# Optimization experiments

Measured on AMD Instinct MI355X. Metric: run time of the kernel, lower is better.

## Reference

```python
import jax, jax.numpy as jnp
import numpy as np
from functools import partial

IMAGE_SIZE = 256
ORIG_SIZE = 1024
NEAR, FAR = 0.1, 100.0
CHUNK = 100  # faces processed per scan step to bound memory


def setup_inputs():
    key = jax.random.key(0)
    kv, kf = jax.random.split(key)
    B, V, F = 4, 5000, 10000
    verts = jax.random.normal(kv, (B, V, 3), jnp.float32) * 0.4
    verts = verts.at[..., 2].add(2.5)  # object in front of camera (+z)
    faces = jax.random.randint(kf, (B, F, 3), 0, V)
    fx = fy = float(ORIG_SIZE)
    cx = cy = ORIG_SIZE / 2.0
    K = jnp.broadcast_to(jnp.array([[fx, 0., cx], [0., fy, cy], [0., 0., 1.]], jnp.float32), (B, 3, 3))
    R = jnp.broadcast_to(jnp.eye(3, dtype=jnp.float32), (B, 3, 3))
    t = jnp.zeros((B, 1, 3), jnp.float32)
    dist_coeffs = jnp.zeros((B, 5), jnp.float32)
    return {"vertices": verts, "faces": faces, "K": K, "R": R, "t": t, "dist_coeffs": dist_coeffs}


def projection(vertices, K, R, t, dist_coeffs, orig_size, eps=1e-9):
    # vertices: [B,V,3]; matmul(vertices, R^T) + t, OpenCV distortion, intrinsics, NDC
    v = jnp.einsum('bvj,bij->bvi', vertices, R) + t
    x, y, z = v[..., 0], v[..., 1], v[..., 2]
    x_ = x / (z + eps)
    y_ = y / (z + eps)
    k1, k2, p1, p2, k3 = [dist_coeffs[:, i:i + 1] for i in range(5)]
    r2 = x_ * x_ + y_ * y_
    rad = 1. + k1 * r2 + k2 * r2 * r2 + k3 * r2 * r2 * r2
    x__ = x_ * rad + 2. * p1 * x_ * y_ + p2 * (r2 + 2. * x_ * x_)
    y__ = y_ * rad + p1 * (r2 + 2. * y_ * y_) + 2. * p2 * x_ * y_
    vv = jnp.stack([x__, y__, jnp.ones_like(z)], axis=-1)
    vv = jnp.einsum('bvj,bij->bvi', vv, K)
    u, vc = vv[..., 0], vv[..., 1]
    vc = orig_size - vc  # image y points down
    u = 2. * (u - orig_size / 2.) / orig_size
    vc = 2. * (vc - orig_size / 2.) / orig_size
    return jnp.stack([u, vc, z], axis=-1)  # [B,V,3] in NDC xy, camera z


def vertices_to_faces(vertices, faces):
    # vertices [B,V,3], faces [B,F,3] -> [B,F,3,3]
    return jnp.take_along_axis(vertices[:, :, None, :], faces[:, :, :, None], axis=1)


def rasterize_depth(face_verts, image_size, near, far):
    # face_verts: [B,F,3,3]; z-buffer min of barycentric-interpolated 1/z depth
    B, F = face_verts.shape[:2]
    pad = (-F) % CHUNK
    fv = jnp.pad(face_verts, ((0, 0), (0, pad), (0, 0), (0, 0)))  # padded faces are degenerate
    n_chunks = (F + pad) // CHUNK
    fv = fv.reshape(B, n_chunks, CHUNK, 3, 3).transpose(1, 0, 2, 3, 4)  # [n,B,C,3,3]
    ps = (2. * jnp.arange(image_size, dtype=jnp.float32) + 1. - image_size) / image_size
    xp = ps[None, None, None, :]  # [1,1,1,W]
    yp = ps[None, None, :, None]  # [1,1,H,1]
    eps = 1e-8

    def step(zbuf, chunk):  # chunk [B,C,3,3]
        x = chunk[..., 0]
        y = chunk[..., 1]
        z = chunk[..., 2]
        x0, x1, x2 = (x[..., i, None, None] for i in range(3))
        y0, y1, y2 = (y[..., i, None, None] for i in range(3))
        z0, z1, z2 = (z[..., i, None, None] for i in range(3))
        denom = (y1 - y2) * (x0 - x2) + (x2 - x1) * (y0 - y2)
        ok = jnp.abs(denom) > eps
        safe_d = jnp.where(ok, denom, 1.)
        w0 = ((y1 - y2) * (xp - x2) + (x2 - x1) * (yp - y2)) / safe_d  # [B,C,H,W]
        w1 = ((y2 - y0) * (xp - x2) + (x0 - x2) * (yp - y2)) / safe_d
        w2 = 1. - w0 - w1
        inside = (w0 >= 0.) & (w1 >= 0.) & (w2 >= 0.) & ok
        zs0 = jnp.where(z0 > eps, z0, 1.)
        zs1 = jnp.where(z1 > eps, z1, 1.)
        zs2 = jnp.where(z2 > eps, z2, 1.)
        zinv = w0 / zs0 + w1 / zs1 + w2 / zs2
        zp = 1. / jnp.where(zinv > eps, zinv, 1.)
        valid = inside & (zp > near) & (zp < far) & (z0 > eps) & (z1 > eps) & (z2 > eps)
        zp = jnp.where(valid, zp, far)
        zbuf = jnp.minimum(zbuf, jnp.min(zp, axis=1))  # min over faces in chunk
        return zbuf, None

    zbuf0 = jnp.full((B, image_size, image_size), far, dtype=face_verts.dtype)
    zbuf, _ = jax.lax.scan(step, zbuf0, fv)
    return zbuf[:, ::-1, :]  # flip vertically to image convention


def reference(vertices, faces, K, R, t, dist_coeffs):
    # fill_back: append faces with reversed winding
    faces_fb = jnp.concatenate([faces, faces[:, :, ::-1]], axis=1)
    v_ndc = projection(vertices, K, R, t, dist_coeffs, float(ORIG_SIZE))
    fverts = vertices_to_faces(v_ndc, faces_fb)  # [B,2F,3,3]
    return rasterize_depth(fverts, IMAGE_SIZE, NEAR, FAR)  # [B,H,W] depth map
```

## Files before the change

### kernel.cpp

```cpp
#include <hip/hip_runtime.h>

#define IMG 256
#define TW 32
#define TH 32
#define TILES 64
#define SUBSPLIT 16
#define RSUB 8
#define BIGF 1e30f

typedef float v4f __attribute__((ext_vector_type(4)));

__device__ __forceinline__ float ndc(int i) { return (2.0f*i + 1.0f - IMG) * (1.0f/IMG); }

__device__ __forceinline__ void rank_to_tile(int rank, int& tx, int& ty) {
    int k, base;
    if (rank < 4)       { k = 0; base = 0;  }
    else if (rank < 16) { k = 1; base = 4;  }
    else if (rank < 36) { k = 2; base = 16; }
    else                { k = 3; base = 36; }
    int j = rank - base;
    int s = 2*k + 2;
    int seg = j / (s - 1);
    int off = j - seg * (s - 1);
    int lo = 3 - k, hi = 4 + k;
    if      (seg == 0) { tx = lo + off; ty = lo; }
    else if (seg == 1) { tx = hi;       ty = lo + off; }
    else if (seg == 2) { tx = hi - off; ty = hi; }
    else               { tx = lo;       ty = hi - off; }
}

__device__ __forceinline__ bool tile_test(v4f gx, v4f gy, v4f a,
                                          float txlo, float txhi, float tylo, float tyhi) {
    float m0 = fmaxf(gx.x*txlo, gx.x*txhi) + fmaxf(gy.x*tylo, gy.x*tyhi) + a.x;
    float m1 = fmaxf(gx.y*txlo, gx.y*txhi) + fmaxf(gy.y*tylo, gy.y*tyhi) + a.y;
    float m2 = fmaxf(gx.z*txlo, gx.z*txhi) + fmaxf(gy.z*tylo, gy.z*tyhi) + a.z;
    return fminf(fminf(m0, m1), m2) >= -1e-5f;
}

__device__ __forceinline__ float plane_min(float gw, float hw, float aw,
                                           float xlo, float xhi, float ylo, float yhi) {
    return fminf(gw*xlo, gw*xhi) + fminf(hw*ylo, hw*yhi) + aw;
}

__device__ __forceinline__ float wave_max_dpp(float v) {
    int x;
    x = __builtin_amdgcn_update_dpp(0, __float_as_int(v), 0x111, 0xF, 0xF, true);
    v = fmaxf(v, __int_as_float(x));
    x = __builtin_amdgcn_update_dpp(0, __float_as_int(v), 0x112, 0xF, 0xF, true);
    v = fmaxf(v, __int_as_float(x));
    x = __builtin_amdgcn_update_dpp(0, __float_as_int(v), 0x114, 0xF, 0xF, true);
    v = fmaxf(v, __int_as_float(x));
    x = __builtin_amdgcn_update_dpp(0, __float_as_int(v), 0x118, 0xF, 0xF, true);
    v = fmaxf(v, __int_as_float(x));
    x = __builtin_amdgcn_update_dpp(0, __float_as_int(v), 0x142, 0xF, 0xF, true);
    v = fmaxf(v, __int_as_float(x));
    x = __builtin_amdgcn_update_dpp(0, __float_as_int(v), 0x143, 0xF, 0xF, true);
    v = fmaxf(v, __int_as_float(x));
    return __int_as_float(__builtin_amdgcn_readlane(__float_as_int(v), 63));
}

__device__ __forceinline__ unsigned long long cover_mask_px(int i0, int i1, int j0, int j1,
                                                            v4f gx, v4f gy, v4f aa) {
    if (i0 > 255 || i1 < 0 || j0 > 255 || j1 < 0) return 0ull;
    int tx0 = max(i0, 0) >> 5, tx1 = min(i1, 255) >> 5;
    int ty0 = max(j0, 0) >> 5, ty1 = min(j1, 255) >> 5;
    unsigned long long m = 0ull;
    for (int ty = ty0; ty <= ty1; ++ty) {
        float tylo = ndc(ty*TH), tyhi = ndc(ty*TH + TH - 1);
        for (int tx = tx0; tx <= tx1; ++tx) {
            if (tile_test(gx, gy, aa, ndc(tx*TW), ndc(tx*TW + TW - 1), tylo, tyhi))
                m |= 1ull << (ty*8 + tx);
        }
    }
    return m;
}

__global__ void k_prep(const float* __restrict__ verts, const int* __restrict__ faces,
                       const float* __restrict__ Km, const float* __restrict__ Rm,
                       const float* __restrict__ tm, const float* __restrict__ dm,
                       v4f* __restrict__ fd, v4f* __restrict__ bb,
                       unsigned int* __restrict__ ids,
                       unsigned int* __restrict__ outz, unsigned int* __restrict__ gcnt,
                       int B, int V, int F, int nz, int faceBlocks, int doBins) {
    if ((int)blockIdx.x >= faceBlocks) {
        int idx = (blockIdx.x - faceBlocks) * 256 + threadIdx.x;
        int stride = (gridDim.x - faceBlocks) * 256;
        for (int j = idx; j < nz; j += stride) outz[j] = 0x42C80000u;
        return;
    }
    __shared__ int lcnt[1024];
    __shared__ unsigned int lbase[1024];
    __shared__ int lofs[1024];
    int nbins = TILES * B;
    int tid = threadIdx.x;
    if (doBins) {
        for (int k = tid; k < nbins; k += 256) { lcnt[k] = 0; lofs[k] = 0; }
        __syncthreads();
    }
    int i = blockIdx.x * 256 + tid;
    bool alive = i < B * F;
    unsigned long long tmask = 0ull;
    int b = 0, j0c = 0, j1c = 0;
    if (alive) {
        b = i / F;
        const float* vb = verts + (size_t)b * V * 3;
        const float* R = Rm + b * 9;
        const float* K = Km + b * 9;
        const float* t = tm + b * 3;
        const float* d = dm + b * 5;
        float X[3], Y[3], Z[3];
        #pragma unroll
        for (int c = 0; c < 3; ++c) {
            int vi = faces[3*i + c];
            float px = vb[3*vi], py = vb[3*vi+1], pz = vb[3*vi+2];
            float x = R[0]*px + R[1]*py + R[2]*pz + t[0];
            float y = R[3]*px + R[4]*py + R[5]*pz + t[1];
            float z = R[6]*px + R[7]*py + R[8]*pz + t[2];
            float iz = 1.0f / (z + 1e-9f);
            float x_ = x * iz, y_ = y * iz;
            float k1 = d[0], k2 = d[1], p1 = d[2], p2 = d[3], k3 = d[4];
            float r2 = x_*x_ + y_*y_;
            float rad = 1.0f + k1*r2 + k2*r2*r2 + k3*r2*r2*r2;
            float xd = x_*rad + 2.0f*p1*x_*y_ + p2*(r2 + 2.0f*x_*x_);
            float yd = y_*rad + p1*(r2 + 2.0f*y_*y_) + 2.0f*p2*x_*y_;
            float u  = K[0]*xd + K[1]*yd + K[2];
            float vc = K[3]*xd + K[4]*yd + K[5];
            vc = 1024.0f - vc;
            X[c] = (u  - 512.0f) * (1.0f/512.0f);
            Y[c] = (vc - 512.0f) * (1.0f/512.0f);
            Z[c] = z;
        }
        float x0=X[0], y0=Y[0], z0=Z[0], x1=X[1], y1=Y[1], z1=Z[1], x2=X[2], y2=Y[2], z2=Z[2];
        float denom = (y1-y2)*(x0-x2) + (x2-x1)*(y0-y2);
        bool ok = (fabsf(denom) > 1e-8f) && (z0 > 1e-8f) && (z1 > 1e-8f) && (z2 > 1e-8f);
        if (!ok) {
            bb[i] = (v4f){3e38f, -3e38f, 3e38f, -3e38f};
        } else {
            float s = (denom > 0.0f) ? 1.0f : -1.0f;
            float absd = fabsf(denom);
            float P0x = s*(y1-y2), P0y = s*(x2-x1);
            float P1x = s*(y2-y0), P1y = s*(x0-x2);
            float P2x = -(P0x + P1x), P2y = -(P0y + P1y);
            float A0 = -(P0x*x2 + P0y*y2);
            float A1 = -(P1x*x2 + P1y*y2);
            float A2 = absd - A0 - A1;
            float ia  = 1.0f / absd;
            float rz0 = ia / z0, rz1 = ia / z1, rz2 = ia / z2;
            float zix = P0x*rz0 + P1x*rz1 + P2x*rz2;
            float ziy = P0y*rz0 + P1y*rz1 + P2y*rz2;
            float zic = A0*rz0 + A1*rz1 + A2*rz2;
            v4f ga = (v4f){P0x, P1x, P2x, -zix};
            v4f gb = (v4f){P0y, P1y, P2y, -ziy};
            v4f gc = (v4f){A0,  A1,  A2,  10.0f - zic};
            fd[(size_t)i*3 + 0] = ga;
            fd[(size_t)i*3 + 1] = gb;
            fd[(size_t)i*3 + 2] = gc;
            float xmn = fminf(x0, fminf(x1, x2)) - 1e-4f;
            float xmx = fmaxf(x0, fmaxf(x1, x2)) + 1e-4f;
            float ymn = fminf(y0, fminf(y1, y2)) - 1e-4f;
            float ymx = fmaxf(y0, fmaxf(y1, y2)) + 1e-4f;
            bb[i] = (v4f){xmn, xmx, ymn, ymx};
            if (doBins) {
                int i0 = (int)floorf(xmn*128.0f + 127.5f);
                int i1 = (int)ceilf (xmx*128.0f + 127.5f);
                int j0 = (int)floorf(ymn*128.0f + 127.5f);
                int j1 = (int)ceilf (ymx*128.0f + 127.5f);
                tmask = cover_mask_px(i0, i1, j0, j1, ga, gb, gc);
                j0c = max(j0, 0); j1c = min(j1, 255);
            }
        }
    }
    if (doBins) {
        unsigned long long mk = tmask;
        while (mk) {
            int t = __builtin_ctzll(mk); mk &= mk - 1ull;
            atomicAdd(&lcnt[t*B + b], 1);
        }
        __syncthreads();
        for (int k = tid; k < nbins; k += 256)
            if (lcnt[k]) lbase[k] = atomicAdd(&gcnt[k], (unsigned int)lcnt[k]);
        __syncthreads();
        mk = tmask;
        while (mk) {
            int t = __builtin_ctzll(mk); mk &= mk - 1ull;
            int ty = t >> 3;
            int bin = t*B + b;
            unsigned int blo = (unsigned int)max((j0c >> 3) - ty*4, 0);
            unsigned int bhi = (unsigned int)min((j1c >> 3) - ty*4, 3);
            unsigned int pack = (unsigned int)i | (blo << 28) | (bhi << 30);
            int sl = atomicAdd(&lofs[bin], 1);
            ids[(size_t)bin*F + lbase[bin] + sl] = pack;
        }
    }
}

__global__ __launch_bounds__(256) void k_raster(const v4f* __restrict__ fd,
                                                const unsigned int* __restrict__ ids,
                                                const unsigned int* __restrict__ gcnt,
                                                unsigned int* __restrict__ outz,
                                                int B, int F) {
    __shared__ v4f sA[257], sB[257], sC[257];
    int tid = threadIdx.x, lane = tid & 63, wave = tid >> 6;
    int wbase = wave << 6;
    int tbIdx = blockIdx.x >> 3;
    int sub = blockIdx.x & (RSUB-1);
    int rank = tbIdx / B;
    int b = tbIdx - rank * B;
    int tx, ty;
    rank_to_tile(rank, tx, ty);
    int bin = (ty*8 + tx)*B + b;
    unsigned int len = gcnt[bin];
    size_t base = (size_t)bin * F;
    unsigned int p0 = (unsigned int)(((unsigned long long)sub     * len) / RSUB);
    unsigned int p1 = (unsigned int)(((unsigned long long)(sub+1) * len) / RSUB);

    int rowbase = ty*TH + wave*8;
    int row = rowbase + (lane >> 3);
    int col = tx*TW + (lane & 7) * 4;
    float yp = ndc(row);
    float xp[4];
    #pragma unroll
    for (int jj = 0; jj < 4; ++jj) xp[jj] = ndc(col + jj);
    float txlo = ndc(tx*TW), txhi = ndc(tx*TW + TW - 1);
    float bylo = ndc(rowbase), byhi = ndc(rowbase + 7);
    float m[4] = {BIGF, BIGF, BIGF, BIGF};

    int orow = IMG - 1 - row;
    size_t zo = (size_t)b * (IMG*IMG) + (size_t)orow * IMG + col;

    float hs = 0.0f;
    #pragma unroll
    for (int jj = 0; jj < 4; ++jj) {
        float d = __uint_as_float(outz[zo + jj]);
        hs = fmaxf(hs, 10.0f - 1.0f/d);
    }
    float h = fminf(9.99f, wave_max_dpp(hs) + 1e-4f);

    if (p1 > p0) {
        unsigned int pc = ids[base + min(p0 + lane, p1 - 1)];
        bool vc = (p0 + lane) < p1;
        unsigned int pn = ids[base + min(p0 + 64 + lane, p1 - 1)];
        bool vn = (p0 + 64 + lane) < p1;

        for (unsigned int p = p0; p < p1; p += 64) {
            unsigned int p2w = ids[base + min(p + 128 + lane, p1 - 1)];
            bool v2 = (p + 128 + lane) < p1;

            unsigned int blo = (pc >> 28) & 3u, bhi = pc >> 30;
            unsigned int idc = pc & 0x0FFFFFFFu;
            bool pass = vc & ((int)blo <= wave) & ((int)bhi >= wave);
            bool full = false;
            v4f ra = (v4f){0,0,0,0}, rb = (v4f){0,0,0,0}, rc = (v4f){0,0,0,0};
            if (pass) {
                ra = fd[(size_t)idc*3]; rb = fd[(size_t)idc*3+1]; rc = fd[(size_t)idc*3+2];
                float p0l=ra.x*txlo, p0h=ra.x*txhi, q0l=rb.x*bylo, q0h=rb.x*byhi;
                float p1l=ra.y*txlo, p1h=ra.y*txhi, q1l=rb.y*bylo, q1h=rb.y*byhi;
                float p2l=ra.z*txlo, p2h=ra.z*txhi, q2l=rb.z*bylo, q2h=rb.z*byhi;
                float c0x = fmaxf(p0l,p0h) + fmaxf(q0l,q0h) + rc.x;
                float c1x = fmaxf(p1l,p1h) + fmaxf(q1l,q1h) + rc.y;
                float c2x = fmaxf(p2l,p2h) + fmaxf(q2l,q2h) + rc.z;
                float c0n = fminf(p0l,p0h) + fminf(q0l,q0h) + rc.x;
                float c1n = fminf(p1l,p1h) + fminf(q1l,q1h) + rc.y;
                float c2n = fminf(p2l,p2h) + fminf(q2l,q2h) + rc.z;
                float zmn = fminf(ra.w*txlo, ra.w*txhi) + fminf(rb.w*bylo, rb.w*byhi) + rc.w;
                pass = (fminf(fminf(c0x, c1x), c2x) >= -1e-5f) & (zmn < h);
                full = (fminf(fminf(c0n, c1n), c2n) >= 1e-5f);
            }
            unsigned long long mp = __ballot(pass && !full);
            unsigned long long mf = __ballot(pass && full);
            int cp = __popcll(mp);
            int cf = __popcll(mf);
            if (pass && !full) {
                int sl = wbase + __popcll(mp & ((1ull << lane) - 1ull));
                sA[sl] = ra; sB[sl] = rb; sC[sl] = rc;
            }
            unsigned long long w = mf;
            while (w) {
                int l = __builtin_amdgcn_readfirstlane(__ffsll((unsigned long long)w) - 1);
                w &= w - 1ull;
                float gxw = __int_as_float(__builtin_amdgcn_readlane(__float_as_int(ra.w), l));
                float gyw = __int_as_float(__builtin_amdgcn_readlane(__float_as_int(rb.w), l));
                float aaw = __int_as_float(__builtin_amdgcn_readlane(__float_as_int(rc.w), l));
                float e3 = fmaf(gyw, yp, aaw);
                #pragma unroll
                for (int jj = 0; jj < 4; ++jj)
                    m[jj] = fminf(m[jj], fmaf(gxw, xp[jj], e3));
            }
            if (cp > 0) {
                v4f gx = sA[wbase], gy = sB[wbase], aa = sC[wbase];
                for (int i = 0; i < cp; ++i) {
                    v4f nx = sA[wbase+i+1], ny = sB[wbase+i+1], nzv = sC[wbase+i+1];
                    float e0 = fmaf(gy.x, yp, aa.x);
                    float e1 = fmaf(gy.y, yp, aa.y);
                    float e2 = fmaf(gy.z, yp, aa.z);
                    float e3 = fmaf(gy.w, yp, aa.w);
                    #pragma unroll
                    for (int jj = 0; jj < 4; ++jj) {
                        float n0 = fmaf(gx.x, xp[jj], e0);
                        float n1 = fmaf(gx.y, xp[jj], e1);
                        float n2 = fmaf(gx.z, xp[jj], e2);
                        float n3 = fmaf(gx.w, xp[jj], e3);
                        float q = fminf(fminf(n0, n1), n2);
                        m[jj] = fminf(m[jj], (q >= 0.0f) ? n3 : BIGF);
                    }
                    gx = nx; gy = ny; aa = nzv;
                }
            }
            if (cp + cf > 0)
                h = fminf(9.99f, wave_max_dpp(fmaxf(fmaxf(m[0], m[1]), fmaxf(m[2], m[3]))));
            pc = pn; vc = vn;
            pn = p2w; vn = v2;
        }
    }
    #pragma unroll
    for (int jj = 0; jj < 4; ++jj) {
        if (m[jj] < 9.99f) {
            float depth = 1.0f / (10.0f - m[jj]);
            unsigned int mv = __float_as_uint(depth);
            unsigned int cv = outz[zo + jj];
            if (mv < cv) atomicMin(&outz[zo + jj], mv);
        }
    }
}

__global__ __launch_bounds__(256) void k_raster_scan(const v4f* __restrict__ fd,
                                                     const v4f* __restrict__ bb,
                                                     unsigned int* __restrict__ outz,
                                                     int B, int F) {
    __shared__ v4f sA[257], sB[257], sC[257];
    int tid = threadIdx.x, lane = tid & 63, wave = tid >> 6;
    int wbase = wave << 6;
    int j = blockIdx.x >> 4;
    int s = blockIdx.x & (SUBSPLIT-1);
    int nTB = TILES * B;
    int f_begin = (s * F) / SUBSPLIT, f_end = ((s + 1) * F) / SUBSPLIT;

    #pragma unroll 1
    for (int phase = 0; phase < 2; ++phase) {
        int tb = (phase == 0) ? j : (nTB - 1 - j);
        int rank = tb / B;
        int b = tb - rank * B;
        int tx, ty;
        rank_to_tile(rank, tx, ty);
        int rowbase = ty*TH + wave*8;
        int row = rowbase + (lane >> 3);
        int col = tx*TW + (lane & 7) * 4;
        float yp = ndc(row);
        float xp[4];
        #pragma unroll
        for (int jj = 0; jj < 4; ++jj) xp[jj] = ndc(col + jj);
        float txlo = ndc(tx*TW), txhi = ndc(tx*TW + TW - 1);
        float bylo = ndc(rowbase), byhi = ndc(rowbase + 7);
        float m[4] = {BIGF, BIGF, BIGF, BIGF};
        float h = 9.99f;

        const v4f* bbp = bb + (size_t)b * F;
        const v4f* fdp = fd + (size_t)b * F * 3;

        v4f box = bbp[min(f_begin + lane, f_end - 1)];
        bool valid = (f_begin + lane) < f_end;

        for (int g0 = f_begin; g0 < f_end; g0 += 64) {
            int fn = g0 + 64 + lane;
            v4f nbox = bbp[min(fn, f_end - 1)];
            bool nvalid = fn < f_end;

            bool pass = valid &
                        (box.x <= txhi) & (box.y >= txlo) &
                        (box.z <= byhi) & (box.w >= bylo);
            v4f ra, rb, rc;
            if (pass) {
                int f = g0 + lane;
                ra = fdp[3*f]; rb = fdp[3*f+1]; rc = fdp[3*f+2];
                pass = tile_test(ra, rb, rc, txlo, txhi, bylo, byhi)
                    && (plane_min(ra.w, rb.w, rc.w, txlo, txhi, bylo, byhi) < h);
            }
            unsigned long long mk = __ballot(pass);
            int total = __popcll(mk);
            if (pass) {
                int slot = wbase + __popcll(mk & ((1ull << lane) - 1ull));
                sA[slot] = ra;
                sB[slot] = rb;
                sC[slot] = rc;
            }
            if (total > 0) {
                v4f gx = sA[wbase], gy = sB[wbase], aa = sC[wbase];
                for (int i = 0; i < total; ++i) {
                    v4f nx = sA[wbase+i+1], ny = sB[wbase+i+1], nzv = sC[wbase+i+1];
                    float e0 = fmaf(gy.x, yp, aa.x);
                    float e1 = fmaf(gy.y, yp, aa.y);
                    float e2 = fmaf(gy.z, yp, aa.z);
                    float e3 = fmaf(gy.w, yp, aa.w);
                    #pragma unroll
                    for (int jj = 0; jj < 4; ++jj) {
                        float n0 = fmaf(gx.x, xp[jj], e0);
                        float n1 = fmaf(gx.y, xp[jj], e1);
                        float n2 = fmaf(gx.z, xp[jj], e2);
                        float n3 = fmaf(gx.w, xp[jj], e3);
                        float q = fminf(fminf(n0, n1), n2);
                        m[jj] = fminf(m[jj], (q >= 0.0f) ? n3 : BIGF);
                    }
                    gx = nx; gy = ny; aa = nzv;
                }
                h = fminf(9.99f, wave_max_dpp(fmaxf(fmaxf(m[0], m[1]), fmaxf(m[2], m[3]))));
            }
            box = nbox; valid = nvalid;
        }
        int orow = IMG - 1 - row;
        size_t zo = (size_t)b * (IMG*IMG) + (size_t)orow * IMG + col;
        #pragma unroll
        for (int jj = 0; jj < 4; ++jj) {
            if (m[jj] < 9.99f) {
                float depth = 1.0f / (10.0f - m[jj]);
                unsigned int mv = __float_as_uint(depth);
                unsigned int cv = outz[zo + jj];
                if (mv < cv) atomicMin(&outz[zo + jj], mv);
            }
        }
    }
}

extern "C" void kernel_launch(void* const* d_in, const int* in_sizes, int n_in,
                              void* d_out, int out_size, void* d_ws, size_t ws_size,
                              hipStream_t stream) {
    const float* verts = (const float*)d_in[0];
    const int*   faces = (const int*)d_in[1];
    const float* Km    = (const float*)d_in[2];
    const float* Rm    = (const float*)d_in[3];
    const float* tm    = (const float*)d_in[4];
    const float* dm    = (const float*)d_in[5];
    float* out = (float*)d_out;

    int B = in_sizes[2] / 9;
    int V = in_sizes[0] / (3 * B);
    int F = in_sizes[1] / (3 * B);
    int nz = B * IMG * IMG;
    int nbins = TILES * B;

    char* ws = (char*)d_ws;
    size_t al = 255;
    size_t o_fd  = 0;
    size_t o_bb  = (o_fd + (size_t)B*F*48 + al) & ~al;
    size_t o_cnt = (o_bb + (size_t)B*F*16 + al) & ~al;
    size_t o_ids = (o_cnt + (size_t)nbins*4 + al) & ~al;
    size_t need_bins = o_ids + (size_t)nbins * F * 4;
    size_t need_scan = o_ids;

    v4f* fd  = (v4f*)(ws + o_fd);
    v4f* bbp = (v4f*)(ws + o_bb);
    unsigned int* gcnt = (unsigned int*)(ws + o_cnt);
    unsigned int* ids  = (unsigned int*)(ws + o_ids);

    const int thr = 256;
    int faceBlocks = (B*F + thr - 1) / thr;

    if (ws_size >= need_bins && nbins <= 1024 && (size_t)B*F < (1u<<28)) {
        hipMemsetAsync(gcnt, 0, (size_t)nbins*4, stream);
        k_prep<<<faceBlocks + 128, thr, 0, stream>>>(verts, faces, Km, Rm, tm, dm,
                                                     fd, bbp, ids, (unsigned int*)out, gcnt,
                                                     B, V, F, nz, faceBlocks, 1);
        int rasterBlocks = nbins * RSUB;
        k_raster<<<rasterBlocks, thr, 0, stream>>>(fd, ids, gcnt,
                                                   (unsigned int*)out, B, F);
    } else if (ws_size >= need_scan) {
        k_prep<<<faceBlocks + 128, thr, 0, stream>>>(verts, faces, Km, Rm, tm, dm,
                                                     fd, bbp, ids, (unsigned int*)out, gcnt,
                                                     B, V, F, nz, faceBlocks, 0);
        int rasterBlocks = (TILES * B / 2) * SUBSPLIT;
        k_raster_scan<<<rasterBlocks, thr, 0, stream>>>(fd, bbp, (unsigned int*)out, B, F);
    }
}
```

Baseline: 116.4 us.

## Load-balance raster work with a scheduled unit table per bin

Adds a single-block scheduling kernel that prefix-sums per-bin face counts into a table of fixed-size work units of about 256 faces each. The raster kernel then loops grid-stride over these units instead of giving every tile-batch bin a fixed 8-way split, and the spiral tile ordering is dropped. The goal is to even out load when bins hold very different face counts and to avoid launching blocks for empty bins. In exchange it adds an extra serial kernel launch and loses the center-first ordering, which previously helped the depth-based early rejection.

```diff
diff --git a/kernel.cpp b/kernel.cpp
--- a/kernel.cpp
+++ b/kernel.cpp
@@ -5,29 +5,12 @@
 #define TH 32
 #define TILES 64
 #define SUBSPLIT 16
-#define RSUB 8
+#define UNITC 256
 #define BIGF 1e30f
 
 typedef float v4f __attribute__((ext_vector_type(4)));
 
 __device__ __forceinline__ float ndc(int i) { return (2.0f*i + 1.0f - IMG) * (1.0f/IMG); }
-
-__device__ __forceinline__ void rank_to_tile(int rank, int& tx, int& ty) {
-    int k, base;
-    if (rank < 4)       { k = 0; base = 0;  }
-    else if (rank < 16) { k = 1; base = 4;  }
-    else if (rank < 36) { k = 2; base = 16; }
-    else                { k = 3; base = 36; }
-    int j = rank - base;
-    int s = 2*k + 2;
-    int seg = j / (s - 1);
-    int off = j - seg * (s - 1);
-    int lo = 3 - k, hi = 4 + k;
-    if      (seg == 0) { tx = lo + off; ty = lo; }
-    else if (seg == 1) { tx = hi;       ty = lo + off; }
-    else if (seg == 2) { tx = hi - off; ty = hi; }
-    else               { tx = lo;       ty = hi - off; }
-}
 
 __device__ __forceinline__ bool tile_test(v4f gx, v4f gy, v4f a,
                                           float txlo, float txhi, float tylo, float tyhi) {
@@ -194,131 +177,171 @@
     }
 }
 
+__global__ __launch_bounds__(256) void k_sched(const unsigned int* __restrict__ gcnt,
+                                               unsigned int* __restrict__ table,
+                                               unsigned int* __restrict__ nUnits,
+                                               int nbins) {
+    __shared__ unsigned int ps[256];
+    int tid = threadIdx.x;
+    unsigned int loc[4], s = 0;
+    #pragma unroll
+    for (int k = 0; k < 4; ++k) {
+        int idx = tid*4 + k;
+        unsigned int len = (idx < nbins) ? gcnt[idx] : 0u;
+        unsigned int nu = len ? min(255u, (len + UNITC - 1) / UNITC) : 0u;
+        loc[k] = nu; s += nu;
+    }
+    ps[tid] = s; __syncthreads();
+    #pragma unroll
+    for (int d = 1; d < 256; d <<= 1) {
+        unsigned int t = (tid >= d) ? ps[tid - d] : 0u;
+        __syncthreads();
+        ps[tid] += t;
+        __syncthreads();
+    }
+    unsigned int run = ps[tid] - s;
+    #pragma unroll
+    for (int k = 0; k < 4; ++k) {
+        int idx = tid*4 + k;
+        if (idx < nbins) {
+            for (unsigned int j = 0; j < loc[k]; ++j) table[run + j] = ((unsigned int)idx << 8) | j;
+            run += loc[k];
+        }
+    }
+    if (tid == 255) nUnits[0] = ps[255];
+}
+
 __global__ __launch_bounds__(256) void k_raster(const v4f* __restrict__ fd,
                                                 const unsigned int* __restrict__ ids,
                                                 const unsigned int* __restrict__ gcnt,
+                                                const unsigned int* __restrict__ table,
+                                                const unsigned int* __restrict__ nUnits,
                                                 unsigned int* __restrict__ outz,
                                                 int B, int F) {
     __shared__ v4f sA[257], sB[257], sC[257];
     int tid = threadIdx.x, lane = tid & 63, wave = tid >> 6;
     int wbase = wave << 6;
-    int tbIdx = blockIdx.x >> 3;
-    int sub = blockIdx.x & (RSUB-1);
-    int rank = tbIdx / B;
-    int b = tbIdx - rank * B;
-    int tx, ty;
-    rank_to_tile(rank, tx, ty);
-    int bin = (ty*8 + tx)*B + b;
-    unsigned int len = gcnt[bin];
-    size_t base = (size_t)bin * F;
-    unsigned int p0 = (unsigned int)(((unsigned long long)sub     * len) / RSUB);
-    unsigned int p1 = (unsigned int)(((unsigned long long)(sub+1) * len) / RSUB);
-
-    int rowbase = ty*TH + wave*8;
-    int row = rowbase + (lane >> 3);
-    int col = tx*TW + (lane & 7) * 4;
-    float yp = ndc(row);
-    float xp[4];
-    #pragma unroll
-    for (int jj = 0; jj < 4; ++jj) xp[jj] = ndc(col + jj);
-    float txlo = ndc(tx*TW), txhi = ndc(tx*TW + TW - 1);
-    float bylo = ndc(rowbase), byhi = ndc(rowbase + 7);
-    float m[4] = {BIGF, BIGF, BIGF, BIGF};
-
-    int orow = IMG - 1 - row;
-    size_t zo = (size_t)b * (IMG*IMG) + (size_t)orow * IMG + col;
-
-    float hs = 0.0f;
-    #pragma unroll
-    for (int jj = 0; jj < 4; ++jj) {
-        float d = __uint_as_float(outz[zo + jj]);
-        hs = fmaxf(hs, 10.0f - 1.0f/d);
-    }
-    float h = fminf(9.99f, wave_max_dpp(hs) + 1e-4f);
-
-    if (p1 > p0) {
-        unsigned int pc = ids[base + min(p0 + lane, p1 - 1)];
-        bool vc = (p0 + lane) < p1;
-        unsigned int pn = ids[base + min(p0 + 64 + lane, p1 - 1)];
-        bool vn = (p0 + 64 + lane) < p1;
-
-        for (unsigned int p = p0; p < p1; p += 64) {
-            unsigned int p2w = ids[base + min(p + 128 + lane, p1 - 1)];
-            bool v2 = (p + 128 + lane) < p1;
-
-            unsigned int blo = (pc >> 28) & 3u, bhi = pc >> 30;
-            unsigned int idc = pc & 0x0FFFFFFFu;
-            bool pass = vc & ((int)blo <= wave) & ((int)bhi >= wave);
-            bool full = false;
-            v4f ra = (v4f){0,0,0,0}, rb = (v4f){0,0,0,0}, rc = (v4f){0,0,0,0};
-            if (pass) {
-                ra = fd[(size_t)idc*3]; rb = fd[(size_t)idc*3+1]; rc = fd[(size_t)idc*3+2];
-                float p0l=ra.x*txlo, p0h=ra.x*txhi, q0l=rb.x*bylo, q0h=rb.x*byhi;
-                float p1l=ra.y*txlo, p1h=ra.y*txhi, q1l=rb.y*bylo, q1h=rb.y*byhi;
-                float p2l=ra.z*txlo, p2h=ra.z*txhi, q2l=rb.z*bylo, q2h=rb.z*byhi;
-                float c0x = fmaxf(p0l,p0h) + fmaxf(q0l,q0h) + rc.x;
-                float c1x = fmaxf(p1l,p1h) + fmaxf(q1l,q1h) + rc.y;
-                float c2x = fmaxf(p2l,p2h) + fmaxf(q2l,q2h) + rc.z;
-                float c0n = fminf(p0l,p0h) + fminf(q0l,q0h) + rc.x;
-                float c1n = fminf(p1l,p1h) + fminf(q1l,q1h) + rc.y;
-                float c2n = fminf(p2l,p2h) + fminf(q2l,q2h) + rc.z;
-                float zmn = fminf(ra.w*txlo, ra.w*txhi) + fminf(rb.w*bylo, rb.w*byhi) + rc.w;
-                pass = (fminf(fminf(c0x, c1x), c2x) >= -1e-5f) & (zmn < h);
-                full = (fminf(fminf(c0n, c1n), c2n) >= 1e-5f);
-            }
-            unsigned long long mp = __ballot(pass && !full);
-            unsigned long long mf = __ballot(pass && full);
-            int cp = __popcll(mp);
-            int cf = __popcll(mf);
-            if (pass && !full) {
-                int sl = wbase + __popcll(mp & ((1ull << lane) - 1ull));
-                sA[sl] = ra; sB[sl] = rb; sC[sl] = rc;
-            }
-            unsigned long long w = mf;
-            while (w) {
-                int l = __builtin_amdgcn_readfirstlane(__ffsll((unsigned long long)w) - 1);
-                w &= w - 1ull;
-                float gxw = __int_as_float(__builtin_amdgcn_readlane(__float_as_int(ra.w), l));
-                float gyw = __int_as_float(__builtin_amdgcn_readlane(__float_as_int(rb.w), l));
-                float aaw = __int_as_float(__builtin_amdgcn_readlane(__float_as_int(rc.w), l));
-                float e3 = fmaf(gyw, yp, aaw);
-                #pragma unroll
-                for (int jj = 0; jj < 4; ++jj)
-                    m[jj] = fminf(m[jj], fmaf(gxw, xp[jj], e3));
-            }
-            if (cp > 0) {
-                v4f gx = sA[wbase], gy = sB[wbase], aa = sC[wbase];
-                for (int i = 0; i < cp; ++i) {
-                    v4f nx = sA[wbase+i+1], ny = sB[wbase+i+1], nzv = sC[wbase+i+1];
-                    float e0 = fmaf(gy.x, yp, aa.x);
-                    float e1 = fmaf(gy.y, yp, aa.y);
-                    float e2 = fmaf(gy.z, yp, aa.z);
-                    float e3 = fmaf(gy.w, yp, aa.w);
+    unsigned int nU = nUnits[0];
+
+    for (unsigned int u = blockIdx.x; u < nU; u += gridDim.x) {
+        unsigned int entry = table[u];
+        int bin = entry >> 8;
+        unsigned int k = entry & 255u;
+        int t = bin / B;
+        int b = bin - t * B;
+        int ty = t >> 3, tx = t & 7;
+        unsigned int len = gcnt[bin];
+        unsigned int nu = min(255u, (len + UNITC - 1) / UNITC);
+        size_t base = (size_t)bin * F;
+        unsigned int p0 = (unsigned int)(((unsigned long long)k     * len) / nu);
+        unsigned int p1 = (unsigned int)(((unsigned long long)(k+1) * len) / nu);
+
+        int rowbase = ty*TH + wave*8;
+        int row = rowbase + (lane >> 3);
+        int col = tx*TW + (lane & 7) * 4;
+        float yp = ndc(row);
+        float xp[4];
+        #pragma unroll
+        for (int jj = 0; jj < 4; ++jj) xp[jj] = ndc(col + jj);
+        float txlo = ndc(tx*TW), txhi = ndc(tx*TW + TW - 1);
+        float bylo = ndc(rowbase), byhi = ndc(rowbase + 7);
+        float m[4] = {BIGF, BIGF, BIGF, BIGF};
+
+        int orow = IMG - 1 - row;
+        size_t zo = (size_t)b * (IMG*IMG) + (size_t)orow * IMG + col;
+
+        float hs = 0.0f;
+        #pragma unroll
+        for (int jj = 0; jj < 4; ++jj) {
+            float d = __uint_as_float(outz[zo + jj]);
+            hs = fmaxf(hs, 10.0f - 1.0f/d);
+        }
+        float h = fminf(9.99f, wave_max_dpp(hs) + 1e-4f);
+
+        if (p1 > p0) {
+            unsigned int pc = ids[base + min(p0 + lane, p1 - 1)];
+            bool vc = (p0 + lane) < p1;
+            unsigned int pn = ids[base + min(p0 + 64 + lane, p1 - 1)];
+            bool vn = (p0 + 64 + lane) < p1;
+
+            for (unsigned int p = p0; p < p1; p += 64) {
+                unsigned int p2w = ids[base + min(p + 128 + lane, p1 - 1)];
+                bool v2 = (p + 128 + lane) < p1;
+
+                unsigned int blo = (pc >> 28) & 3u, bhi = pc >> 30;
+                unsigned int idc = pc & 0x0FFFFFFFu;
+                bool pass = vc & ((int)blo <= wave) & ((int)bhi >= wave);
+                bool full = false;
+                v4f ra = (v4f){0,0,0,0}, rb = (v4f){0,0,0,0}, rc = (v4f){0,0,0,0};
+                if (pass) {
+                    ra = fd[(size_t)idc*3]; rb = fd[(size_t)idc*3+1]; rc = fd[(size_t)idc*3+2];
+                    float p0l=ra.x*txlo, p0h=ra.x*txhi, q0l=rb.x*bylo, q0h=rb.x*byhi;
+                    float p1l=ra.y*txlo, p1h=ra.y*txhi, q1l=rb.y*bylo, q1h=rb.y*byhi;
+                    float p2l=ra.z*txlo, p2h=ra.z*txhi, q2l=rb.z*bylo, q2h=rb.z*byhi;
+                    float c0x = fmaxf(p0l,p0h) + fmaxf(q0l,q0h) + rc.x;
+                    float c1x = fmaxf(p1l,p1h) + fmaxf(q1l,q1h) + rc.y;
+                    float c2x = fmaxf(p2l,p2h) + fmaxf(q2l,q2h) + rc.z;
+                    float c0n = fminf(p0l,p0h) + fminf(q0l,q0h) + rc.x;
+                    float c1n = fminf(p1l,p1h) + fminf(q1l,q1h) + rc.y;
+                    float c2n = fminf(p2l,p2h) + fminf(q2l,q2h) + rc.z;
+                    float zmn = fminf(ra.w*txlo, ra.w*txhi) + fminf(rb.w*bylo, rb.w*byhi) + rc.w;
+                    pass = (fminf(fminf(c0x, c1x), c2x) >= -1e-5f) & (zmn < h);
+                    full = (fminf(fminf(c0n, c1n), c2n) >= 1e-5f);
+                }
+                unsigned long long mp = __ballot(pass && !full);
+                unsigned long long mf = __ballot(pass && full);
+                int cp = __popcll(mp);
+                int cf = __popcll(mf);
+                if (pass && !full) {
+                    int sl = wbase + __popcll(mp & ((1ull << lane) - 1ull));
+                    sA[sl] = ra; sB[sl] = rb; sC[sl] = rc;
+                }
+                unsigned long long w = mf;
+                while (w) {
+                    int l = __builtin_amdgcn_readfirstlane(__ffsll((unsigned long long)w) - 1);
+                    w &= w - 1ull;
+                    float gxw = __int_as_float(__builtin_amdgcn_readlane(__float_as_int(ra.w), l));
+                    float gyw = __int_as_float(__builtin_amdgcn_readlane(__float_as_int(rb.w), l));
+                    float aaw = __int_as_float(__builtin_amdgcn_readlane(__float_as_int(rc.w), l));
+                    float e3 = fmaf(gyw, yp, aaw);
                     #pragma unroll
-                    for (int jj = 0; jj < 4; ++jj) {
-                        float n0 = fmaf(gx.x, xp[jj], e0);
-                        float n1 = fmaf(gx.y, xp[jj], e1);
-                        float n2 = fmaf(gx.z, xp[jj], e2);
-                        float n3 = fmaf(gx.w, xp[jj], e3);
-                        float q = fminf(fminf(n0, n1), n2);
-                        m[jj] = fminf(m[jj], (q >= 0.0f) ? n3 : BIGF);
+                    for (int jj = 0; jj < 4; ++jj)
+                        m[jj] = fminf(m[jj], fmaf(gxw, xp[jj], e3));
+                }
+                if (cp > 0) {
+                    v4f gx = sA[wbase], gy = sB[wbase], aa = sC[wbase];
+                    for (int i = 0; i < cp; ++i) {
+                        v4f nx = sA[wbase+i+1], ny = sB[wbase+i+1], nzv = sC[wbase+i+1];
+                        float e0 = fmaf(gy.x, yp, aa.x);
+                        float e1 = fmaf(gy.y, yp, aa.y);
+                        float e2 = fmaf(gy.z, yp, aa.z);
+                        float e3 = fmaf(gy.w, yp, aa.w);
+                        #pragma unroll
+                        for (int jj = 0; jj < 4; ++jj) {
+                            float n0 = fmaf(gx.x, xp[jj], e0);
+                            float n1 = fmaf(gx.y, xp[jj], e1);
+                            float n2 = fmaf(gx.z, xp[jj], e2);
+                            float n3 = fmaf(gx.w, xp[jj], e3);
+                            float q = fminf(fminf(n0, n1), n2);
+                            m[jj] = fminf(m[jj], (q >= 0.0f) ? n3 : BIGF);
+                        }
+                        gx = nx; gy = ny; aa = nzv;
                     }
-                    gx = nx; gy = ny; aa = nzv;
                 }
-            }
-            if (cp + cf > 0)
-                h = fminf(9.99f, wave_max_dpp(fmaxf(fmaxf(m[0], m[1]), fmaxf(m[2], m[3]))));
-            pc = pn; vc = vn;
-            pn = p2w; vn = v2;
-        }
-    }
-    #pragma unroll
-    for (int jj = 0; jj < 4; ++jj) {
-        if (m[jj] < 9.99f) {
-            float depth = 1.0f / (10.0f - m[jj]);
-            unsigned int mv = __float_as_uint(depth);
-            unsigned int cv = outz[zo + jj];
-            if (mv < cv) atomicMin(&outz[zo + jj], mv);
+                if (cp + cf > 0)
+                    h = fminf(9.99f, wave_max_dpp(fmaxf(fmaxf(m[0], m[1]), fmaxf(m[2], m[3]))));
+                pc = pn; vc = vn;
+                pn = p2w; vn = v2;
+            }
+        }
+        #pragma unroll
+        for (int jj = 0; jj < 4; ++jj) {
+            if (m[jj] < 9.99f) {
+                float depth = 1.0f / (10.0f - m[jj]);
+                unsigned int mv = __float_as_uint(depth);
+                unsigned int cv = outz[zo + jj];
+                if (mv < cv) atomicMin(&outz[zo + jj], mv);
+            }
         }
     }
 }
@@ -340,8 +363,7 @@
         int tb = (phase == 0) ? j : (nTB - 1 - j);
         int rank = tb / B;
         int b = tb - rank * B;
-        int tx, ty;
-        rank_to_tile(rank, tx, ty);
+        int tx = rank & 7, ty = rank >> 3;
         int rowbase = ty*TH + wave*8;
         int row = rowbase + (lane >> 3);
         int col = tx*TW + (lane & 7) * 4;
@@ -442,14 +464,18 @@
     size_t o_fd  = 0;
     size_t o_bb  = (o_fd + (size_t)B*F*48 + al) & ~al;
     size_t o_cnt = (o_bb + (size_t)B*F*16 + al) & ~al;
-    size_t o_ids = (o_cnt + (size_t)nbins*4 + al) & ~al;
+    size_t o_tab = (o_cnt + (size_t)nbins*4 + al) & ~al;
+    size_t o_nu  = (o_tab + (size_t)nbins*255*4 + al) & ~al;
+    size_t o_ids = (o_nu + 256 + al) & ~al;
     size_t need_bins = o_ids + (size_t)nbins * F * 4;
-    size_t need_scan = o_ids;
+    size_t need_scan = o_tab;
 
     v4f* fd  = (v4f*)(ws + o_fd);
     v4f* bbp = (v4f*)(ws + o_bb);
-    unsigned int* gcnt = (unsigned int*)(ws + o_cnt);
-    unsigned int* ids  = (unsigned int*)(ws + o_ids);
+    unsigned int* gcnt   = (unsigned int*)(ws + o_cnt);
+    unsigned int* table  = (unsigned int*)(ws + o_tab);
+    unsigned int* nUnits = (unsigned int*)(ws + o_nu);
+    unsigned int* ids    = (unsigned int*)(ws + o_ids);
 
     const int thr = 256;
     int faceBlocks = (B*F + thr - 1) / thr;
@@ -459,9 +485,9 @@
         k_prep<<<faceBlocks + 128, thr, 0, stream>>>(verts, faces, Km, Rm, tm, dm,
                                                      fd, bbp, ids, (unsigned int*)out, gcnt,
                                                      B, V, F, nz, faceBlocks, 1);
-        int rasterBlocks = nbins * RSUB;
-        k_raster<<<rasterBlocks, thr, 0, stream>>>(fd, ids, gcnt,
-                                                   (unsigned int*)out, B, F);
+        k_sched<<<1, thr, 0, stream>>>(gcnt, table, nUnits, nbins);
+        k_raster<<<2048, thr, 0, stream>>>(fd, ids, gcnt, table, nUnits,
+                                           (unsigned int*)out, B, F);
     } else if (ws_size >= need_scan) {
         k_prep<<<faceBlocks + 128, thr, 0, stream>>>(verts, faces, Km, Rm, tm, dm,
                                                      fd, bbp, ids, (unsigned int*)out, gcnt,
```

New measurement: 122.7 us. 5.4% more time.

## Precompute per-band occluder depth bound in prep to seed raster culling threshold

Applied to the files above, without the earlier changes.

During binning, each face that fully covers a tile's column span and all pixels of an 8-row band records a conservative depth bound into a per-band buffer via atomicMin. The raster kernel uses this bound to seed its early-out threshold h, so faces behind a known full-coverage occluder can be culled from the start instead of waiting for the running z-buffer to tighten. It adds extra per-face work and global atomics in the prep kernel, plus an extra memset. The update rule for h is also changed to keep the tighter of the old and new values.

```diff
diff --git a/kernel.cpp b/kernel.cpp
--- a/kernel.cpp
+++ b/kernel.cpp
@@ -79,7 +79,7 @@
                        const float* __restrict__ Km, const float* __restrict__ Rm,
                        const float* __restrict__ tm, const float* __restrict__ dm,
                        v4f* __restrict__ fd, v4f* __restrict__ bb,
-                       unsigned int* __restrict__ ids,
+                       unsigned int* __restrict__ ids, unsigned int* __restrict__ bandH,
                        unsigned int* __restrict__ outz, unsigned int* __restrict__ gcnt,
                        int B, int V, int F, int nz, int faceBlocks, int doBins) {
     if ((int)blockIdx.x >= faceBlocks) {
@@ -100,7 +100,8 @@
     int i = blockIdx.x * 256 + tid;
     bool alive = i < B * F;
     unsigned long long tmask = 0ull;
-    int b = 0, j0c = 0, j1c = 0;
+    int b = 0, i0c = 0, i1c = 0, j0c = 0, j1c = 0;
+    v4f ga, gb, gc;
     if (alive) {
         b = i / F;
         const float* vb = verts + (size_t)b * V * 3;
@@ -149,9 +150,9 @@
             float zix = P0x*rz0 + P1x*rz1 + P2x*rz2;
             float ziy = P0y*rz0 + P1y*rz1 + P2y*rz2;
             float zic = A0*rz0 + A1*rz1 + A2*rz2;
-            v4f ga = (v4f){P0x, P1x, P2x, -zix};
-            v4f gb = (v4f){P0y, P1y, P2y, -ziy};
-            v4f gc = (v4f){A0,  A1,  A2,  10.0f - zic};
+            ga = (v4f){P0x, P1x, P2x, -zix};
+            gb = (v4f){P0y, P1y, P2y, -ziy};
+            gc = (v4f){A0,  A1,  A2,  10.0f - zic};
             fd[(size_t)i*3 + 0] = ga;
             fd[(size_t)i*3 + 1] = gb;
             fd[(size_t)i*3 + 2] = gc;
@@ -166,6 +167,7 @@
                 int j0 = (int)floorf(ymn*128.0f + 127.5f);
                 int j1 = (int)ceilf (ymx*128.0f + 127.5f);
                 tmask = cover_mask_px(i0, i1, j0, j1, ga, gb, gc);
+                i0c = max(i0, 0); i1c = min(i1, 255);
                 j0c = max(j0, 0); j1c = min(j1, 255);
             }
         }
@@ -183,13 +185,30 @@
         mk = tmask;
         while (mk) {
             int t = __builtin_ctzll(mk); mk &= mk - 1ull;
-            int ty = t >> 3;
+            int ty = t >> 3, tx = t & 7;
             int bin = t*B + b;
             unsigned int blo = (unsigned int)max((j0c >> 3) - ty*4, 0);
             unsigned int bhi = (unsigned int)min((j1c >> 3) - ty*4, 3);
             unsigned int pack = (unsigned int)i | (blo << 28) | (bhi << 30);
             int sl = atomicAdd(&lofs[bin], 1);
             ids[(size_t)bin*F + lbase[bin] + sl] = pack;
+            if (i0c <= tx*TW && i1c >= tx*TW + TW - 1) {
+                float txlo = ndc(tx*TW), txhi = ndc(tx*TW + TW - 1);
+                float p0n = fminf(ga.x*txlo, ga.x*txhi);
+                float p1n = fminf(ga.y*txlo, ga.y*txhi);
+                float p2n = fminf(ga.z*txlo, ga.z*txhi);
+                float pzx = fmaxf(ga.w*txlo, ga.w*txhi);
+                for (int w = (int)blo; w <= (int)bhi; ++w) {
+                    float bylo = ndc(ty*TH + w*8), byhi = ndc(ty*TH + w*8 + 7);
+                    float c0n = p0n + fminf(gb.x*bylo, gb.x*byhi) + gc.x;
+                    float c1n = p1n + fminf(gb.y*bylo, gb.y*byhi) + gc.y;
+                    float c2n = p2n + fminf(gb.z*bylo, gb.z*byhi) + gc.z;
+                    if (fminf(fminf(c0n, c1n), c2n) >= 1e-5f) {
+                        float bmax = pzx + fmaxf(gb.w*bylo, gb.w*byhi) + gc.w;
+                        atomicMin(&bandH[bin*4 + w], __float_as_uint(bmax));
+                    }
+                }
+            }
         }
     }
 }
@@ -197,6 +216,7 @@
 __global__ __launch_bounds__(256) void k_raster(const v4f* __restrict__ fd,
                                                 const unsigned int* __restrict__ ids,
                                                 const unsigned int* __restrict__ gcnt,
+                                                const unsigned int* __restrict__ bandH,
                                                 unsigned int* __restrict__ outz,
                                                 int B, int F) {
     __shared__ v4f sA[257], sB[257], sC[257];
@@ -228,13 +248,14 @@
     int orow = IMG - 1 - row;
     size_t zo = (size_t)b * (IMG*IMG) + (size_t)orow * IMG + col;
 
+    float hb = __uint_as_float(bandH[bin*4 + wave]);
     float hs = 0.0f;
     #pragma unroll
     for (int jj = 0; jj < 4; ++jj) {
         float d = __uint_as_float(outz[zo + jj]);
         hs = fmaxf(hs, 10.0f - 1.0f/d);
     }
-    float h = fminf(9.99f, wave_max_dpp(hs) + 1e-4f);
+    float h = fminf(fminf(9.99f, hb + 1e-4f), wave_max_dpp(hs) + 1e-4f);
 
     if (p1 > p0) {
         unsigned int pc = ids[base + min(p0 + lane, p1 - 1)];
@@ -307,7 +328,7 @@
                 }
             }
             if (cp + cf > 0)
-                h = fminf(9.99f, wave_max_dpp(fmaxf(fmaxf(m[0], m[1]), fmaxf(m[2], m[3]))));
+                h = fminf(h, wave_max_dpp(fmaxf(fmaxf(m[0], m[1]), fmaxf(m[2], m[3]))));
             pc = pn; vc = vn;
             pn = p2w; vn = v2;
         }
@@ -442,29 +463,34 @@
     size_t o_fd  = 0;
     size_t o_bb  = (o_fd + (size_t)B*F*48 + al) & ~al;
     size_t o_cnt = (o_bb + (size_t)B*F*16 + al) & ~al;
-    size_t o_ids = (o_cnt + (size_t)nbins*4 + al) & ~al;
+    size_t o_bh  = (o_cnt + (size_t)nbins*4 + al) & ~al;
+    size_t o_ids = (o_bh + (size_t)nbins*16 + al) & ~al;
     size_t need_bins = o_ids + (size_t)nbins * F * 4;
-    size_t need_scan = o_ids;
+    size_t need_scan = o_bh;
 
     v4f* fd  = (v4f*)(ws + o_fd);
     v4f* bbp = (v4f*)(ws + o_bb);
-    unsigned int* gcnt = (unsigned int*)(ws + o_cnt);
-    unsigned int* ids  = (unsigned int*)(ws + o_ids);
+    unsigned int* gcnt  = (unsigned int*)(ws + o_cnt);
+    unsigned int* bandH = (unsigned int*)(ws + o_bh);
+    unsigned int* ids   = (unsigned int*)(ws + o_ids);
 
     const int thr = 256;
     int faceBlocks = (B*F + thr - 1) / thr;
 
     if (ws_size >= need_bins && nbins <= 1024 && (size_t)B*F < (1u<<28)) {
         hipMemsetAsync(gcnt, 0, (size_t)nbins*4, stream);
+        hipMemsetAsync(bandH, 0x7F, (size_t)nbins*16, stream);
         k_prep<<<faceBlocks + 128, thr, 0, stream>>>(verts, faces, Km, Rm, tm, dm,
-                                                     fd, bbp, ids, (unsigned int*)out, gcnt,
+                                                     fd, bbp, ids, bandH,
+                                                     (unsigned int*)out, gcnt,
                                                      B, V, F, nz, faceBlocks, 1);
         int rasterBlocks = nbins * RSUB;
-        k_raster<<<rasterBlocks, thr, 0, stream>>>(fd, ids, gcnt,
+        k_raster<<<rasterBlocks, thr, 0, stream>>>(fd, ids, gcnt, bandH,
                                                    (unsigned int*)out, B, F);
     } else if (ws_size >= need_scan) {
         k_prep<<<faceBlocks + 128, thr, 0, stream>>>(verts, faces, Km, Rm, tm, dm,
-                                                     fd, bbp, ids, (unsigned int*)out, gcnt,
+                                                     fd, bbp, ids, bandH,
+                                                     (unsigned int*)out, gcnt,
                                                      B, V, F, nz, faceBlocks, 0);
         int rasterBlocks = (TILES * B / 2) * SUBSPLIT;
         k_raster_scan<<<rasterBlocks, thr, 0, stream>>>(fd, bbp, (unsigned int*)out, B, F);
```

Result: slower. 184.8 us (+58.8%).

## Split tile bins into near and far face classes for earlier depth culling

Applied to the files above, without the earlier changes.

Each face is classified by its nearest vertex depth into near or far classes. The two classes are written from opposite ends of each bin's id array, and the raster kernel processes near faces first, then far faces. Processing near faces first should tighten the per-wave depth bound h early, so more far faces can be skipped by the existing hierarchical cull. The running bound is now kept monotone across segments with fminf(h, ...). This doubles the shared-memory counters and global bin counts and adds a second loop pass per block.

```diff
diff --git a/kernel.cpp b/kernel.cpp
--- a/kernel.cpp
+++ b/kernel.cpp
@@ -6,6 +6,7 @@
 #define TILES 64
 #define SUBSPLIT 16
 #define RSUB 8
+#define ZTHR 9.5f
 #define BIGF 1e30f
 
 typedef float v4f __attribute__((ext_vector_type(4)));
@@ -88,19 +89,19 @@
         for (int j = idx; j < nz; j += stride) outz[j] = 0x42C80000u;
         return;
     }
-    __shared__ int lcnt[1024];
-    __shared__ unsigned int lbase[1024];
-    __shared__ int lofs[1024];
+    __shared__ int lcnt[2048];
+    __shared__ unsigned int lbase[2048];
+    __shared__ int lofs[2048];
     int nbins = TILES * B;
     int tid = threadIdx.x;
     if (doBins) {
-        for (int k = tid; k < nbins; k += 256) { lcnt[k] = 0; lofs[k] = 0; }
+        for (int k = tid; k < 2*nbins; k += 256) { lcnt[k] = 0; lofs[k] = 0; }
         __syncthreads();
     }
     int i = blockIdx.x * 256 + tid;
     bool alive = i < B * F;
     unsigned long long tmask = 0ull;
-    int b = 0, j0c = 0, j1c = 0;
+    int b = 0, j0c = 0, j1c = 0, cls = 0;
     if (alive) {
         b = i / F;
         const float* vb = verts + (size_t)b * V * 3;
@@ -109,6 +110,7 @@
         const float* t = tm + b * 3;
         const float* d = dm + b * 5;
         float X[3], Y[3], Z[3];
+        float maxzi = 0.0f;
         #pragma unroll
         for (int c = 0; c < 3; ++c) {
             int vi = faces[3*i + c];
@@ -117,6 +119,7 @@
             float y = R[3]*px + R[4]*py + R[5]*pz + t[1];
             float z = R[6]*px + R[7]*py + R[8]*pz + t[2];
             float iz = 1.0f / (z + 1e-9f);
+            maxzi = fmaxf(maxzi, iz);
             float x_ = x * iz, y_ = y * iz;
             float k1 = d[0], k2 = d[1], p1 = d[2], p2 = d[3], k3 = d[4];
             float r2 = x_*x_ + y_*y_;
@@ -167,6 +170,7 @@
                 int j1 = (int)ceilf (ymx*128.0f + 127.5f);
                 tmask = cover_mask_px(i0, i1, j0, j1, ga, gb, gc);
                 j0c = max(j0, 0); j1c = min(j1, 255);
+                cls = ((10.0f - maxzi) < ZTHR) ? 0 : 1;
             }
         }
     }
@@ -174,10 +178,10 @@
         unsigned long long mk = tmask;
         while (mk) {
             int t = __builtin_ctzll(mk); mk &= mk - 1ull;
-            atomicAdd(&lcnt[t*B + b], 1);
+            atomicAdd(&lcnt[(t*B + b)*2 + cls], 1);
         }
         __syncthreads();
-        for (int k = tid; k < nbins; k += 256)
+        for (int k = tid; k < 2*nbins; k += 256)
             if (lcnt[k]) lbase[k] = atomicAdd(&gcnt[k], (unsigned int)lcnt[k]);
         __syncthreads();
         mk = tmask;
@@ -188,8 +192,12 @@
             unsigned int blo = (unsigned int)max((j0c >> 3) - ty*4, 0);
             unsigned int bhi = (unsigned int)min((j1c >> 3) - ty*4, 3);
             unsigned int pack = (unsigned int)i | (blo << 28) | (bhi << 30);
-            int sl = atomicAdd(&lofs[bin], 1);
-            ids[(size_t)bin*F + lbase[bin] + sl] = pack;
+            int key = bin*2 + cls;
+            int sl = atomicAdd(&lofs[key], 1);
+            unsigned int pos = lbase[key] + (unsigned int)sl;
+            size_t idx = (cls == 0) ? ((size_t)bin*F + pos)
+                                    : ((size_t)bin*F + (F - 1) - pos);
+            ids[idx] = pack;
         }
     }
 }
@@ -209,10 +217,9 @@
     int tx, ty;
     rank_to_tile(rank, tx, ty);
     int bin = (ty*8 + tx)*B + b;
-    unsigned int len = gcnt[bin];
+    unsigned int lnN = gcnt[bin*2 + 0];
+    unsigned int lnF = gcnt[bin*2 + 1];
     size_t base = (size_t)bin * F;
-    unsigned int p0 = (unsigned int)(((unsigned long long)sub     * len) / RSUB);
-    unsigned int p1 = (unsigned int)(((unsigned long long)(sub+1) * len) / RSUB);
 
     int rowbase = ty*TH + wave*8;
     int row = rowbase + (lane >> 3);
@@ -236,7 +243,14 @@
     }
     float h = fminf(9.99f, wave_max_dpp(hs) + 1e-4f);
 
-    if (p1 > p0) {
+    #pragma unroll 1
+    for (int seg = 0; seg < 2; ++seg) {
+        unsigned int segLen = (seg == 0) ? lnN : lnF;
+        unsigned int segOff = (seg == 0) ? 0u : (unsigned int)F - lnF;
+        unsigned int p0 = segOff + (unsigned int)(((unsigned long long)sub     * segLen) / RSUB);
+        unsigned int p1 = segOff + (unsigned int)(((unsigned long long)(sub+1) * segLen) / RSUB);
+        if (p1 <= p0) continue;
+
         unsigned int pc = ids[base + min(p0 + lane, p1 - 1)];
         bool vc = (p0 + lane) < p1;
         unsigned int pn = ids[base + min(p0 + 64 + lane, p1 - 1)];
@@ -307,7 +321,7 @@
                 }
             }
             if (cp + cf > 0)
-                h = fminf(9.99f, wave_max_dpp(fmaxf(fmaxf(m[0], m[1]), fmaxf(m[2], m[3]))));
+                h = fminf(h, wave_max_dpp(fmaxf(fmaxf(m[0], m[1]), fmaxf(m[2], m[3]))));
             pc = pn; vc = vn;
             pn = p2w; vn = v2;
         }
@@ -442,7 +456,7 @@
     size_t o_fd  = 0;
     size_t o_bb  = (o_fd + (size_t)B*F*48 + al) & ~al;
     size_t o_cnt = (o_bb + (size_t)B*F*16 + al) & ~al;
-    size_t o_ids = (o_cnt + (size_t)nbins*4 + al) & ~al;
+    size_t o_ids = (o_cnt + (size_t)nbins*8 + al) & ~al;
     size_t need_bins = o_ids + (size_t)nbins * F * 4;
     size_t need_scan = o_ids;
 
@@ -455,7 +469,7 @@
     int faceBlocks = (B*F + thr - 1) / thr;
 
     if (ws_size >= need_bins && nbins <= 1024 && (size_t)B*F < (1u<<28)) {
-        hipMemsetAsync(gcnt, 0, (size_t)nbins*4, stream);
+        hipMemsetAsync(gcnt, 0, (size_t)nbins*8, stream);
         k_prep<<<faceBlocks + 128, thr, 0, stream>>>(verts, faces, Km, Rm, tm, dm,
                                                      fd, bbp, ids, (unsigned int*)out, gcnt,
                                                      B, V, F, nz, faceBlocks, 1);
```

New measurement: 115.7 us (median of 2 runs). Within noise of the previous version (-0.6%).
